# Optimization experiments

Measured on AMD Instinct MI355X. Metric: run time of the kernel, lower is better.

Reference implementation:

```python
import jax, jax.numpy as jnp
import numpy as np

N_NODES = 50000
N_EDGES = 640000
D = 128
N_GRAPHS = 64
N_CLASSES = 32
N_LAYERS = 4


def setup_inputs() -> dict:
    key = jax.random.key(0)
    ks = jax.random.split(key, 8)
    x = jax.random.normal(ks[0], (N_NODES, D), dtype=jnp.float32)
    edge_index = jax.random.randint(ks[1], (2, N_EDGES), 0, N_NODES, dtype=jnp.int64)
    batch = jnp.sort(jax.random.randint(ks[2], (N_NODES,), 0, N_GRAPHS, dtype=jnp.int64))
    s = 0.05  # small init scale (stand-in for init_weights)
    w1 = jax.random.normal(ks[3], (N_LAYERS, D, D), dtype=jnp.float32) * s
    b1 = jnp.zeros((N_LAYERS, D), dtype=jnp.float32)
    w2 = jax.random.normal(ks[4], (N_LAYERS, D, D), dtype=jnp.float32) * s
    b2 = jnp.zeros((N_LAYERS, D), dtype=jnp.float32)
    w_lin = jax.random.normal(ks[5], (D, N_CLASSES), dtype=jnp.float32) * s
    b_lin = jnp.zeros((N_CLASSES,), dtype=jnp.float32)
    return {"x": x, "edge_index": edge_index, "batch": batch,
            "w1": w1, "b1": b1, "w2": w2, "b2": b2,
            "w_lin": w_lin, "b_lin": b_lin}


def reference(x, edge_index, batch, w1, b1, w2, b2, w_lin, b_lin):
    # GIN stack: num_layers GINConv layers (eps=0, sum aggregation,
    # MLP = Linear -> ReLU -> Linear), ReLU between layers (not after last).
    src, dst = edge_index[0], edge_index[1]
    n = x.shape[0]
    h = x
    for i in range(N_LAYERS):
        # neighbor sum aggregation: scatter-add messages h[src] into dst
        agg = jax.ops.segment_sum(h[src], dst, num_segments=n)
        z = h + agg  # (1 + eps) * x_i + sum_j x_j, eps = 0
        z = jnp.maximum(z @ w1[i] + b1[i], 0.0)
        h = z @ w2[i] + b2[i]
        if i < N_LAYERS - 1:
            h = jax.nn.relu(h)
    # global_mean_pool over graph ids
    sums = jax.ops.segment_sum(h, batch, num_segments=N_GRAPHS)
    counts = jax.ops.segment_sum(jnp.ones((n,), dtype=h.dtype), batch, num_segments=N_GRAPHS)
    pooled = sums / jnp.maximum(counts, 1.0)[:, None]
    logits = pooled @ w_lin + b_lin
    return (pooled, logits)
```

## Files before the change

kernel.cpp:

```cpp
#include <hip/hip_runtime.h>
#include <hip/hip_fp16.h>


typedef short short8 __attribute__((ext_vector_type(8)));
typedef float floatx4 __attribute__((ext_vector_type(4)));

#define TM 32
#define ZSTRIDE 136

__device__ __forceinline__ unsigned short f2bf(float x) {
    unsigned int u = __float_as_uint(x);
    u += 0x7fffu + ((u >> 16) & 1u);
    return (unsigned short)(u >> 16);
}
__device__ __forceinline__ float bf2f(unsigned short h) {
    return __uint_as_float(((unsigned int)h) << 16);
}

__device__ __forceinline__ float2 ldrowh(const char* __restrict__ base,
                                         int id, unsigned laneoff) {
    __half2 h = *(const __half2*)(base + ((unsigned)id << 8) + laneoff);
    return __half22float2(h);
}


__global__ __launch_bounds__(256) void gin_build1(
    const int* __restrict__ dst, int nEdges, int* __restrict__ counts,
    int* __restrict__ rank,
    const float* __restrict__ w1, const float* __restrict__ w2,
    unsigned short* __restrict__ whf, unsigned short* __restrict__ wlf, int wTotal,
    const float* __restrict__ x, __half* __restrict__ xh, int nNodes) {
    const int gsize = gridDim.x * 256;
    const int gtid = blockIdx.x * 256 + threadIdx.x;
    for (int idx = gtid; idx < wTotal; idx += gsize) {
        int mat  = idx >> 14;
        int rem  = idx & 16383;
        int kc   = rem >> 12;
        int ct   = (rem >> 9) & 7;
        int lane = (rem >> 3) & 63;
        int j    = rem & 7;
        int row = kc * 32 + (lane >> 4) * 8 + j;
        int col = ct * 16 + (lane & 15);
        int L = mat >> 1;
        const float* W = (mat & 1) ? (w2 + (size_t)L * 16384) : (w1 + (size_t)L * 16384);
        float v = W[row * 128 + col];
        unsigned short h = f2bf(v);
        unsigned short l = f2bf(v - bf2f(h));
        whf[idx] = h;
        wlf[idx] = l;
    }
    const int total4 = nNodes * 32;
    for (int i = gtid; i < total4; i += gsize) {
        float4 v = ((const float4*)x)[i];
        union { __half2 h[2]; float2 f; } u;
        u.h[0] = __halves2half2(__float2half_rn(v.x), __float2half_rn(v.y));
        u.h[1] = __halves2half2(__float2half_rn(v.z), __float2half_rn(v.w));
        ((float2*)xh)[i] = u.f;
    }
    for (int i = gtid; i < nEdges; i += gsize)
        rank[i] = atomicAdd(&counts[dst[i]], 1);
}


__global__ __launch_bounds__(256) void gin_scanA(const int* __restrict__ counts,
                                                 int* __restrict__ offsets,
                                                 int* __restrict__ partials, int n) {
    __shared__ int s[256];
    int t = threadIdx.x;
    int i = blockIdx.x * 256 + t;
    int v = (i < n) ? counts[i] : 0;
    s[t] = v;
    __syncthreads();
    for (int off = 1; off < 256; off <<= 1) {
        int u = (t >= off) ? s[t - off] : 0;
        __syncthreads();
        s[t] += u;
        __syncthreads();
    }
    if (i < n) offsets[i] = s[t] - v;
    if (t == 255) partials[blockIdx.x] = s[255];
}


__global__ __launch_bounds__(256) void gin_scanB(int* __restrict__ offsets,
                                                 const int* __restrict__ partials,
                                                 int nb, int n, int nEdges) {
    __shared__ int s[256];
    int t = threadIdx.x;
    s[t] = (t < nb) ? partials[t] : 0;
    __syncthreads();
    for (int off = 1; off < 256; off <<= 1) {
        int u = (t >= off) ? s[t - off] : 0;
        __syncthreads();
        s[t] += u;
        __syncthreads();
    }
    int base = (blockIdx.x > 0) ? s[blockIdx.x - 1] : 0;
    int i = blockIdx.x * 256 + t;
    if (i < n) offsets[i] += base;
    if (i == 0) offsets[n] = nEdges;
}


__global__ __launch_bounds__(256) void gin_scatter(const int* __restrict__ src,
                                                   const int* __restrict__ dst,
                                                   const int* __restrict__ rank,
                                                   int nEdges,
                                                   const int* __restrict__ offsets,
                                                   int* __restrict__ ssrc) {
    int i = blockIdx.x * 256 + threadIdx.x;
    if (i < nEdges) {
        int p = offsets[dst[i]] + rank[i];
        ssrc[p] = src[i];
    }
}


__global__ __launch_bounds__(256) void gin_layer(const __half* __restrict__ hin,
                                                 const int* __restrict__ offs,
                                                 const int* __restrict__ ssrc,
                                                 const unsigned short* __restrict__ whf,
                                                 const unsigned short* __restrict__ wlf,
                                                 int matBase,
                                                 const float* __restrict__ b1p,
                                                 const float* __restrict__ b2p,
                                                 __half* __restrict__ hout,
                                                 const int* __restrict__ batch,
                                                 float* __restrict__ gsums,
                                                 int nNodes, int lastLayer) {
    __shared__ unsigned short smem[2 * TM * ZSTRIDE];
    unsigned short* zh = smem;
    unsigned short* zl = smem + TM * ZSTRIDE;
    const int tid = threadIdx.x;
    const int w = tid >> 6, lane = tid & 63;
    const int lo4 = lane & 15, hi4 = lane >> 4;
    const int rowbase = blockIdx.x * TM;
    const char* hbase = (const char*)hin;
    const unsigned laneoff = (unsigned)lane * 4u;

    const int gbase = rowbase + w * 8;
#pragma unroll
    for (int pp = 0; pp < 4; ++pp) {
        int nA = gbase + 2 * pp, nB = nA + 1;
        bool okA = nA < nNodes, okB = nB < nNodes;
        float2 aA = make_float2(0.f, 0.f), aB = make_float2(0.f, 0.f);
        if (okA) aA = ldrowh(hbase, nA, laneoff);
        if (okB) aB = ldrowh(hbase, nB, laneoff);
        int eA = okA ? offs[nA] : 0, endA = okA ? offs[nA + 1] : 0;
        int eB = okB ? offs[nB] : 0, endB = okB ? offs[nB + 1] : 0;

        while (eA + 4 <= endA && eB + 4 <= endB) {
            int sA0 = ssrc[eA], sA1 = ssrc[eA + 1], sA2 = ssrc[eA + 2], sA3 = ssrc[eA + 3];
            int sB0 = ssrc[eB], sB1 = ssrc[eB + 1], sB2 = ssrc[eB + 2], sB3 = ssrc[eB + 3];
            float2 vA0 = ldrowh(hbase, sA0, laneoff);
            float2 vA1 = ldrowh(hbase, sA1, laneoff);
            float2 vA2 = ldrowh(hbase, sA2, laneoff);
            float2 vA3 = ldrowh(hbase, sA3, laneoff);
            float2 vB0 = ldrowh(hbase, sB0, laneoff);
            float2 vB1 = ldrowh(hbase, sB1, laneoff);
            float2 vB2 = ldrowh(hbase, sB2, laneoff);
            float2 vB3 = ldrowh(hbase, sB3, laneoff);
            aA.x += (vA0.x + vA1.x) + (vA2.x + vA3.x);
            aA.y += (vA0.y + vA1.y) + (vA2.y + vA3.y);
            aB.x += (vB0.x + vB1.x) + (vB2.x + vB3.x);
            aB.y += (vB0.y + vB1.y) + (vB2.y + vB3.y);
            eA += 4; eB += 4;
        }
        for (; eA + 4 <= endA; eA += 4) {
            int s0 = ssrc[eA], s1 = ssrc[eA + 1], s2 = ssrc[eA + 2], s3 = ssrc[eA + 3];
            float2 v0 = ldrowh(hbase, s0, laneoff);
            float2 v1 = ldrowh(hbase, s1, laneoff);
            float2 v2 = ldrowh(hbase, s2, laneoff);
            float2 v3 = ldrowh(hbase, s3, laneoff);
            aA.x += (v0.x + v1.x) + (v2.x + v3.x);
            aA.y += (v0.y + v1.y) + (v2.y + v3.y);
        }
        for (; eA < endA; ++eA) {
            float2 v = ldrowh(hbase, ssrc[eA], laneoff);
            aA.x += v.x; aA.y += v.y;
        }
        for (; eB + 4 <= endB; eB += 4) {
            int s0 = ssrc[eB], s1 = ssrc[eB + 1], s2 = ssrc[eB + 2], s3 = ssrc[eB + 3];
            float2 v0 = ldrowh(hbase, s0, laneoff);
            float2 v1 = ldrowh(hbase, s1, laneoff);
            float2 v2 = ldrowh(hbase, s2, laneoff);
            float2 v3 = ldrowh(hbase, s3, laneoff);
            aB.x += (v0.x + v1.x) + (v2.x + v3.x);
            aB.y += (v0.y + v1.y) + (v2.y + v3.y);
        }
        for (; eB < endB; ++eB) {
            float2 v = ldrowh(hbase, ssrc[eB], laneoff);
            aB.x += v.x; aB.y += v.y;
        }
        int rA = nA - rowbase, rB = rA + 1;
        unsigned short hx = f2bf(aA.x), hy = f2bf(aA.y);
        ((unsigned int*)zh)[rA * (ZSTRIDE / 2) + lane] = (unsigned)hx | ((unsigned)hy << 16);
        ((unsigned int*)zl)[rA * (ZSTRIDE / 2) + lane] =
            (unsigned)f2bf(aA.x - bf2f(hx)) | ((unsigned)f2bf(aA.y - bf2f(hy)) << 16);
        hx = f2bf(aB.x); hy = f2bf(aB.y);
        ((unsigned int*)zh)[rB * (ZSTRIDE / 2) + lane] = (unsigned)hx | ((unsigned)hy << 16);
        ((unsigned int*)zl)[rB * (ZSTRIDE / 2) + lane] =
            (unsigned)f2bf(aB.x - bf2f(hx)) | ((unsigned)f2bf(aB.y - bf2f(hy)) << 16);
    }
    __syncthreads();

    floatx4 acc[2][2];
#pragma unroll
    for (int rg = 0; rg < 2; ++rg)
#pragma unroll
        for (int ct = 0; ct < 2; ++ct) acc[rg][ct] = (floatx4)0.f;

    for (int kc = 0; kc < 4; ++kc) {
        size_t o0 = ((((size_t)matBase * 4 + kc) * 8 + (2 * w)) * 64 + lane) * 8;
        size_t o1 = ((((size_t)matBase * 4 + kc) * 8 + (2 * w + 1)) * 64 + lane) * 8;
        short8 bh0 = *(const short8*)(whf + o0), bl0 = *(const short8*)(wlf + o0);
        short8 bh1 = *(const short8*)(whf + o1), bl1 = *(const short8*)(wlf + o1);
#pragma unroll
        for (int rg = 0; rg < 2; ++rg) {
            const int rbase = (rg * 16 + lo4) * ZSTRIDE + kc * 32 + hi4 * 8;
            short8 ah = *(const short8*)(zh + rbase);
            short8 al = *(const short8*)(zl + rbase);
            acc[rg][0] = __builtin_amdgcn_mfma_f32_16x16x32_bf16(ah, bh0, acc[rg][0], 0, 0, 0);
            acc[rg][0] = __builtin_amdgcn_mfma_f32_16x16x32_bf16(al, bh0, acc[rg][0], 0, 0, 0);
            acc[rg][0] = __builtin_amdgcn_mfma_f32_16x16x32_bf16(ah, bl0, acc[rg][0], 0, 0, 0);
            acc[rg][1] = __builtin_amdgcn_mfma_f32_16x16x32_bf16(ah, bh1, acc[rg][1], 0, 0, 0);
            acc[rg][1] = __builtin_amdgcn_mfma_f32_16x16x32_bf16(al, bh1, acc[rg][1], 0, 0, 0);
            acc[rg][1] = __builtin_amdgcn_mfma_f32_16x16x32_bf16(ah, bl1, acc[rg][1], 0, 0, 0);
        }
    }
    __syncthreads();

    float bb1_0 = b1p[w * 32 + lo4];
    float bb1_1 = b1p[w * 32 + 16 + lo4];
#pragma unroll
    for (int rg = 0; rg < 2; ++rg)
#pragma unroll
        for (int ct = 0; ct < 2; ++ct) {
            float bb = ct ? bb1_1 : bb1_0;
#pragma unroll
            for (int r = 0; r < 4; ++r) {
                float v = fmaxf(acc[rg][ct][r] + bb, 0.f);
                unsigned short h = f2bf(v);
                int idx = (rg * 16 + hi4 * 4 + r) * ZSTRIDE + w * 32 + ct * 16 + lo4;
                zh[idx] = h;
                zl[idx] = f2bf(v - bf2f(h));
            }
        }
    __syncthreads();

#pragma unroll
    for (int rg = 0; rg < 2; ++rg)
#pragma unroll
        for (int ct = 0; ct < 2; ++ct) acc[rg][ct] = (floatx4)0.f;

    for (int kc = 0; kc < 4; ++kc) {
        size_t o0 = ((((size_t)(matBase + 1) * 4 + kc) * 8 + (2 * w)) * 64 + lane) * 8;
        size_t o1 = ((((size_t)(matBase + 1) * 4 + kc) * 8 + (2 * w + 1)) * 64 + lane) * 8;
        short8 bh0 = *(const short8*)(whf + o0), bl0 = *(const short8*)(wlf + o0);
        short8 bh1 = *(const short8*)(whf + o1), bl1 = *(const short8*)(wlf + o1);
#pragma unroll
        for (int rg = 0; rg < 2; ++rg) {
            const int rbase = (rg * 16 + lo4) * ZSTRIDE + kc * 32 + hi4 * 8;
            short8 ah = *(const short8*)(zh + rbase);
            short8 al = *(const short8*)(zl + rbase);
            acc[rg][0] = __builtin_amdgcn_mfma_f32_16x16x32_bf16(ah, bh0, acc[rg][0], 0, 0, 0);
            acc[rg][0] = __builtin_amdgcn_mfma_f32_16x16x32_bf16(al, bh0, acc[rg][0], 0, 0, 0);
            acc[rg][0] = __builtin_amdgcn_mfma_f32_16x16x32_bf16(ah, bl0, acc[rg][0], 0, 0, 0);
            acc[rg][1] = __builtin_amdgcn_mfma_f32_16x16x32_bf16(ah, bh1, acc[rg][1], 0, 0, 0);
            acc[rg][1] = __builtin_amdgcn_mfma_f32_16x16x32_bf16(al, bh1, acc[rg][1], 0, 0, 0);
            acc[rg][1] = __builtin_amdgcn_mfma_f32_16x16x32_bf16(ah, bl1, acc[rg][1], 0, 0, 0);
        }
    }

    float bb2_0 = b2p[w * 32 + lo4];
    float bb2_1 = b2p[w * 32 + 16 + lo4];

    if (!lastLayer) {
#pragma unroll
        for (int rg = 0; rg < 2; ++rg)
#pragma unroll
            for (int ct = 0; ct < 2; ++ct) {
                float bb = ct ? bb2_1 : bb2_0;
#pragma unroll
                for (int r = 0; r < 4; ++r) {
                    int row = rowbase + rg * 16 + hi4 * 4 + r;
                    if (row < nNodes) {
                        float v = fmaxf(acc[rg][ct][r] + bb, 0.f);
                        hout[(size_t)row * 128 + w * 32 + ct * 16 + lo4] = __float2half_rn(v);
                    }
                }
            }
    } else {
        __syncthreads();
        float* zf = (float*)smem;
#pragma unroll
        for (int rg = 0; rg < 2; ++rg)
#pragma unroll
            for (int ct = 0; ct < 2; ++ct) {
                float bb = ct ? bb2_1 : bb2_0;
#pragma unroll
                for (int r = 0; r < 4; ++r)
                    zf[(rg * 16 + hi4 * 4 + r) * 132 + w * 32 + ct * 16 + lo4] =
                        acc[rg][ct][r] + bb;
            }
        __syncthreads();
        int c = tid & 127, half = tid >> 7;
        int rmax = nNodes - rowbase;
        if (rmax > TM) rmax = TM;
        float accp = 0.f;
        int gcur = -1;
        for (int r = half; r < rmax; r += 2) {
            int g = batch[rowbase + r];
            if (g != gcur) {
                if (gcur >= 0) atomicAdd(&gsums[gcur * 128 + c], accp);
                accp = 0.f;
                gcur = g;
            }
            accp += zf[r * 132 + c];
        }
        if (gcur >= 0) atomicAdd(&gsums[gcur * 128 + c], accp);
    }
}


__device__ __forceinline__ int lb_search(const int* __restrict__ a, int n, int key) {
    int lo = 0, hi = n;
    while (lo < hi) {
        int m = (lo + hi) >> 1;
        if (a[m] < key) lo = m + 1; else hi = m;
    }
    return lo;
}

__global__ __launch_bounds__(128) void gin_pool2(const float* __restrict__ gsums,
                                                 const int* __restrict__ batch, int nNodes,
                                                 const float* __restrict__ wlin,
                                                 const float* __restrict__ blin,
                                                 float* __restrict__ out, int nGraphs) {
    __shared__ float sp[128];
    int g = blockIdx.x;
    int t = threadIdx.x;
    int start = lb_search(batch, nNodes, g);
    int end   = lb_search(batch, nNodes, g + 1);
    float cnt = (float)(end - start);
    float p = gsums[(size_t)g * 128 + t] / fmaxf(cnt, 1.0f);
    out[(size_t)g * 128 + t] = p;
    sp[t] = p;
    __syncthreads();
    if (t < 32) {
        float s = blin[t];
        for (int k = 0; k < 128; ++k) s += sp[k] * wlin[k * 32 + t];
        out[(size_t)nGraphs * 128 + g * 32 + t] = s;
    }
}


extern "C" void kernel_launch(void* const* d_in, const int* in_sizes, int n_in,
                              void* d_out, int out_size, void* d_ws, size_t ws_size,
                              hipStream_t stream) {
    const float* x     = (const float*)d_in[0];
    const int*   ei    = (const int*)d_in[1];
    const int*   batch = (const int*)d_in[2];
    const float* w1    = (const float*)d_in[3];
    const float* b1    = (const float*)d_in[4];
    const float* w2    = (const float*)d_in[5];
    const float* b2    = (const float*)d_in[6];
    const float* wlin  = (const float*)d_in[7];
    const float* blin  = (const float*)d_in[8];
    float* out = (float*)d_out;

    const int nNodes  = in_sizes[0] / 128;
    const int nEdges  = in_sizes[1] / 2;
    const int nLayers = in_sizes[3] / (128 * 128);
    const int nGraphs = out_size / 160;

    const int* srcArr = ei;
    const int* dstArr = ei + nEdges;

    char* p = (char*)d_ws;
    int*   counts   = (int*)p;            p += (size_t)nNodes * 4;
    float* gsums    = (float*)p;          p += (size_t)nGraphs * 128 * 4;
    int*   offsets  = (int*)p;            p += (size_t)(nNodes + 1) * 4;
    int*   rank     = (int*)p;            p += (size_t)nEdges * 4;
    int*   partials = (int*)p;            p += 256 * 4;
    int*   ssrc     = (int*)p;            p += (size_t)nEdges * 4;

    p = (char*)(((uintptr_t)p + 63) & ~(uintptr_t)63);
    const int wTotal = nLayers * 2 * 16384;
    unsigned short* whf = (unsigned short*)p;  p += (size_t)wTotal * 2;
    unsigned short* wlf = (unsigned short*)p;  p += (size_t)wTotal * 2;

    p = (char*)(((uintptr_t)p + 63) & ~(uintptr_t)63);
    __half* xh   = (__half*)p;            p += (size_t)nNodes * 128 * 2;
    __half* bufA = (__half*)p;            p += (size_t)nNodes * 128 * 2;
    __half* bufB = (__half*)p;

    const size_t zeroBytes = ((size_t)nNodes + (size_t)nGraphs * 128) * 4;
    hipMemsetAsync(d_ws, 0, zeroBytes, stream);

    const int eb = (nEdges + 255) / 256;
    const int nb = (nNodes + 255) / 256;

    gin_build1<<<eb, 256, 0, stream>>>(dstArr, nEdges, counts, rank, w1, w2,
                                       whf, wlf, wTotal, x, xh, nNodes);
    gin_scanA<<<nb, 256, 0, stream>>>(counts, offsets, partials, nNodes);
    gin_scanB<<<nb, 256, 0, stream>>>(offsets, partials, nb, nNodes, nEdges);
    gin_scatter<<<eb, 256, 0, stream>>>(srcArr, dstArr, rank, nEdges, offsets, ssrc);

    const int lb = (nNodes + TM - 1) / TM;
    const __half* hin = xh;
    __half* bufs[2] = {bufA, bufB};
    for (int L = 0; L < nLayers; ++L) {
        int last = (L == nLayers - 1);
        __half* hout = bufs[L & 1];
        gin_layer<<<lb, 256, 0, stream>>>(hin, offsets, ssrc, whf, wlf, 2 * L,
                                          b1 + (size_t)L * 128, b2 + (size_t)L * 128,
                                          hout, batch, gsums, nNodes, last);
        hin = hout;
    }
    gin_pool2<<<nGraphs, 128, 0, stream>>>(gsums, batch, nNodes, wlin, blin, out, nGraphs);
}
```

Before: 314.1 us.

## Pad edge-count atomics per node and fuse offset finalisation into scatter

New measurement: 312.7 us. No clear change (-0.4%).

```diff
diff --git a/kernel.cpp b/kernel.cpp
--- a/kernel.cpp
+++ b/kernel.cpp
@@ -7,6 +7,7 @@
 
 #define TM 32
 #define ZSTRIDE 136
+#define CSTRIDE 16
 
 __device__ __forceinline__ unsigned short f2bf(float x) {
     unsigned int u = __float_as_uint(x);
@@ -58,17 +59,17 @@
         ((float2*)xh)[i] = u.f;
     }
     for (int i = gtid; i < nEdges; i += gsize)
-        rank[i] = atomicAdd(&counts[dst[i]], 1);
+        rank[i] = atomicAdd(&counts[(size_t)dst[i] * CSTRIDE], 1);
 }
 
 
 __global__ __launch_bounds__(256) void gin_scanA(const int* __restrict__ counts,
-                                                 int* __restrict__ offsets,
+                                                 int* __restrict__ offsLocal,
                                                  int* __restrict__ partials, int n) {
     __shared__ int s[256];
     int t = threadIdx.x;
     int i = blockIdx.x * 256 + t;
-    int v = (i < n) ? counts[i] : 0;
+    int v = (i < n) ? counts[(size_t)i * CSTRIDE] : 0;
     s[t] = v;
     __syncthreads();
     for (int off = 1; off < 256; off <<= 1) {
@@ -77,15 +78,18 @@
         s[t] += u;
         __syncthreads();
     }
-    if (i < n) offsets[i] = s[t] - v;
+    if (i < n) offsLocal[i] = s[t] - v;
     if (t == 255) partials[blockIdx.x] = s[255];
 }
 
 
-__global__ __launch_bounds__(256) void gin_scanB(int* __restrict__ offsets,
-                                                 const int* __restrict__ partials,
-                                                 int nb, int n, int nEdges) {
+__global__ __launch_bounds__(256) void gin_scatfuse(
+    const int* __restrict__ src, const int* __restrict__ dst,
+    const int* __restrict__ rank, int nEdges,
+    const int* __restrict__ offsLocal, const int* __restrict__ partials,
+    int nb, int* __restrict__ offsFinal, int* __restrict__ ssrc, int nNodes) {
     __shared__ int s[256];
+    __shared__ int base[256];
     int t = threadIdx.x;
     s[t] = (t < nb) ? partials[t] : 0;
     __syncthreads();
@@ -95,23 +99,19 @@
         s[t] += u;
         __syncthreads();
     }
-    int base = (blockIdx.x > 0) ? s[blockIdx.x - 1] : 0;
+    base[t] = (t > 0) ? s[t - 1] : 0;
+    __syncthreads();
+
     int i = blockIdx.x * 256 + t;
-    if (i < n) offsets[i] += base;
-    if (i == 0) offsets[n] = nEdges;
-}
-
-
-__global__ __launch_bounds__(256) void gin_scatter(const int* __restrict__ src,
-                                                   const int* __restrict__ dst,
-                                                   const int* __restrict__ rank,
-                                                   int nEdges,
-                                                   const int* __restrict__ offsets,
-                                                   int* __restrict__ ssrc) {
-    int i = blockIdx.x * 256 + threadIdx.x;
     if (i < nEdges) {
-        int p = offsets[dst[i]] + rank[i];
+        int d = dst[i];
+        int p = offsLocal[d] + base[d >> 8] + rank[i];
         ssrc[p] = src[i];
+    }
+    if (blockIdx.x < (unsigned)nb) {
+        int j = blockIdx.x * 256 + t;
+        if (j < nNodes) offsFinal[j] = offsLocal[j] + base[blockIdx.x];
+        if (j == 0) offsFinal[nNodes] = nEdges;
     }
 }
 
@@ -378,12 +378,13 @@
     const int* dstArr = ei + nEdges;
 
     char* p = (char*)d_ws;
-    int*   counts   = (int*)p;            p += (size_t)nNodes * 4;
-    float* gsums    = (float*)p;          p += (size_t)nGraphs * 128 * 4;
-    int*   offsets  = (int*)p;            p += (size_t)(nNodes + 1) * 4;
-    int*   rank     = (int*)p;            p += (size_t)nEdges * 4;
-    int*   partials = (int*)p;            p += 256 * 4;
-    int*   ssrc     = (int*)p;            p += (size_t)nEdges * 4;
+    int*   counts    = (int*)p;           p += (size_t)nNodes * CSTRIDE * 4;
+    float* gsums     = (float*)p;         p += (size_t)nGraphs * 128 * 4;
+    int*   offsLocal = (int*)p;           p += (size_t)(nNodes + 1) * 4;
+    int*   offsFinal = (int*)p;           p += (size_t)(nNodes + 1) * 4;
+    int*   rank      = (int*)p;           p += (size_t)nEdges * 4;
+    int*   partials  = (int*)p;           p += 256 * 4;
+    int*   ssrc      = (int*)p;           p += (size_t)nEdges * 4;
 
     p = (char*)(((uintptr_t)p + 63) & ~(uintptr_t)63);
     const int wTotal = nLayers * 2 * 16384;
@@ -395,7 +396,7 @@
     __half* bufA = (__half*)p;            p += (size_t)nNodes * 128 * 2;
     __half* bufB = (__half*)p;
 
-    const size_t zeroBytes = ((size_t)nNodes + (size_t)nGraphs * 128) * 4;
+    const size_t zeroBytes = ((size_t)nNodes * CSTRIDE + (size_t)nGraphs * 128) * 4;
     hipMemsetAsync(d_ws, 0, zeroBytes, stream);
 
     const int eb = (nEdges + 255) / 256;
@@ -403,9 +404,10 @@
 
     gin_build1<<<eb, 256, 0, stream>>>(dstArr, nEdges, counts, rank, w1, w2,
                                        whf, wlf, wTotal, x, xh, nNodes);
-    gin_scanA<<<nb, 256, 0, stream>>>(counts, offsets, partials, nNodes);
-    gin_scanB<<<nb, 256, 0, stream>>>(offsets, partials, nb, nNodes, nEdges);
-    gin_scatter<<<eb, 256, 0, stream>>>(srcArr, dstArr, rank, nEdges, offsets, ssrc);
+    gin_scanA<<<nb, 256, 0, stream>>>(counts, offsLocal, partials, nNodes);
+    gin_scatfuse<<<eb, 256, 0, stream>>>(srcArr, dstArr, rank, nEdges,
+                                         offsLocal, partials, nb,
+                                         offsFinal, ssrc, nNodes);
 
     const int lb = (nNodes + TM - 1) / TM;
     const __half* hin = xh;
@@ -413,7 +415,7 @@
     for (int L = 0; L < nLayers; ++L) {
         int last = (L == nLayers - 1);
         __half* hout = bufs[L & 1];
-        gin_layer<<<lb, 256, 0, stream>>>(hin, offsets, ssrc, whf, wlf, 2 * L,
+        gin_layer<<<lb, 256, 0, stream>>>(hin, offsFinal, ssrc, whf, wlf, 2 * L,
                                           b1 + (size_t)L * 128, b2 + (size_t)L * 128,
                                           hout, batch, gsums, nNodes, last);
         hin = hout;
```
